# Performance work log

Hardware: AMD Instinct MI355X
Metric: run time of the kernel (lower is better)

Reference implementation:

```python
import jax, jax.numpy as jnp
import numpy as np

CONF_THRES = 0.2   # from __init__ default
IOU_THRES = 0.6    # from __init__ default
MAX_WH = 4096.0    # class-offset for multi-class NMS (yolov7 convention)
TOPK = 2048        # pre-NMS candidates per image
MAX_DET = 300      # max detections per image (yolov7 default)
B, N, NC = 8, 25200, 80


def setup_inputs() -> dict:
    key = jax.random.key(0)
    k1, k2, k3 = jax.random.split(key, 3)
    # decoded predictions: [cx, cy, w, h, obj, cls_0..cls_79]
    xywh = jax.random.uniform(k1, (B, N, 4)) * jnp.array([640.0, 640.0, 120.0, 120.0])
    obj = jax.random.uniform(k2, (B, N, 1))
    cls = jax.random.uniform(k3, (B, N, NC))
    preds = jnp.concatenate([xywh, obj, cls], axis=-1)  # [B, N, 85]
    return {"preds": preds}


def _xywh2xyxy(xywh):
    cx, cy, w, h = xywh[..., 0], xywh[..., 1], xywh[..., 2], xywh[..., 3]
    return jnp.stack([cx - w * 0.5, cy - h * 0.5, cx + w * 0.5, cy + h * 0.5], axis=-1)


def _box_iou(a, b):
    # a: [K,4], b: [K,4] -> [K,K] pairwise IoU
    area_a = (a[:, 2] - a[:, 0]) * (a[:, 3] - a[:, 1])
    area_b = (b[:, 2] - b[:, 0]) * (b[:, 3] - b[:, 1])
    lt = jnp.maximum(a[:, None, :2], b[None, :, :2])  # [K,K,2]
    rb = jnp.minimum(a[:, None, 2:], b[None, :, 2:])
    wh = jnp.clip(rb - lt, 0.0)
    inter = wh[..., 0] * wh[..., 1]
    return inter / (area_a[:, None] + area_b[None, :] - inter + 1e-9)


def _nms_single(pred):
    # pred: [N, 5+NC]
    boxes = _xywh2xyxy(pred[:, :4])                 # [N,4]
    scores_all = pred[:, 5:] * pred[:, 4:5]         # obj * cls  [N,NC]
    conf = jnp.max(scores_all, axis=-1)             # best-class conf
    cls_id = jnp.argmax(scores_all, axis=-1)
    scores = jnp.where(conf > CONF_THRES, conf, 0.0)

    # pre-NMS top-k candidates (sorted descending)
    top_scores, idx = jax.lax.top_k(scores, TOPK)
    top_boxes = boxes[idx]                          # [K,4]
    top_cls = cls_id[idx]                           # [K]
    top_valid = top_scores > CONF_THRES

    # per-class NMS via class offset so cross-class boxes never overlap
    offset_boxes = top_boxes + (top_cls.astype(top_boxes.dtype) * MAX_WH)[:, None]
    iou = _box_iou(offset_boxes, offset_boxes)      # [K,K]

    # greedy NMS over score-sorted candidates
    def body(i, state):
        keep, suppressed = state
        k_i = top_valid[i] & jnp.logical_not(suppressed[i])
        keep = keep.at[i].set(k_i)
        sup_new = suppressed | (k_i & (iou[i] > IOU_THRES))
        sup_new = sup_new.at[i].set(suppressed[i])  # never self-suppress
        return keep, sup_new

    keep, _ = jax.lax.fori_loop(
        0, TOPK, body,
        (jnp.zeros(TOPK, dtype=bool), jnp.zeros(TOPK, dtype=bool)))

    # take top MAX_DET kept detections
    keep_scores = jnp.where(keep, top_scores, -1.0)
    det_scores, det_idx = jax.lax.top_k(keep_scores, MAX_DET)
    det = jnp.concatenate(
        [top_boxes[det_idx],
         det_scores[:, None],
         top_cls[det_idx].astype(pred.dtype)[:, None]], axis=-1)  # [MAX_DET,6]
    det = jnp.where((det_scores > 0.0)[:, None], det, 0.0)
    return det


def reference(preds):
    # preds: [B, N, 5+NC] -> [B, MAX_DET, 6] (x1,y1,x2,y2,conf,cls), zero-padded
    return jax.vmap(_nms_single)(preds)
```

## Files before the change

kernel.cpp:

```cpp
#include <hip/hip_runtime.h>

#define BATCH 8
#define NPRED 25200
#define NCLS 80
#define ROWW 85
#define TOPKK 2048
#define MAXDET 300
#define CANDMAX 4096
#define NBUCKET 4096
#define CONF_T 0.2f
#define IOU_T 0.6f
#define CLS_OFF 4096.0f

#define MASKN 384
#define MCH (MASKN / 64)
#define MW 13

typedef unsigned long long u64;
typedef unsigned int u32;

__device__ __forceinline__ int bucket_of_key(u64 k) {
    float sc = __uint_as_float((u32)(k >> 32));
    int bkt = (int)(sc * (float)NBUCKET);
    return (bkt > NBUCKET - 1) ? (NBUCKET - 1) : bkt;
}

__global__ __launch_bounds__(256) void k_score(
    const float* __restrict__ preds,
    u64* __restrict__ keys,
    unsigned char* __restrict__ cls8,
    u32* __restrict__ hist_g)
{
    __shared__ float rows[64 * ROWW];
    const int t = threadIdx.x;
    const size_t rowbase = (size_t)blockIdx.x * 64;

    const float4* src = reinterpret_cast<const float4*>(preds + rowbase * ROWW);
    float4* dst = reinterpret_cast<float4*>(rows);
    #pragma unroll
    for (int i = t; i < 64 * ROWW / 4; i += 256) dst[i] = src[i];
    __syncthreads();

    const int r = t >> 2;
    const int j = t & 3;
    const float* p = rows + r * ROWW;
    const float obj = p[4];

    float best = -1.0f;
    int bi = 0;
    #pragma unroll
    for (int tt = 0; tt < 20; ++tt) {
        int c = j + 4 * tt;
        float s = __fmul_rn(obj, p[5 + c]);
        if (s > best) { best = s; bi = c; }
    }
    #pragma unroll
    for (int d = 1; d <= 2; d <<= 1) {
        float os = __shfl_xor(best, d);
        int oi = __shfl_xor(bi, d);
        if (os > best || (os == best && oi < bi)) { best = os; bi = oi; }
    }

    if (j == 0) {
        unsigned gid = (unsigned)rowbase + r;
        u64 key = 0ull;
        if (best > CONF_T) {
            key = ((u64)__float_as_uint(best) << 32) | (0xFFFFFFFFu - (gid % NPRED));
        }
        keys[gid] = key;
        cls8[gid] = (unsigned char)bi;
        if (key) {
            atomicAdd(&hist_g[(gid / NPRED) * NBUCKET + bucket_of_key(key)], 1u);
        }
    }
}

__global__ __launch_bounds__(1024) void k_scan(
    const u32* __restrict__ hist_g,
    u32* __restrict__ bstart_g,
    int* __restrict__ tb_g,
    u32* __restrict__ stored_g)
{
    __shared__ u32 wtot[16];
    __shared__ u32 wsuf[16];
    __shared__ int s_tb;
    __shared__ u32 s_stored;

    const int b = blockIdx.x;
    const int t = threadIdx.x;
    const int lane = t & 63;
    const int wave = t >> 6;
    const u32* H = hist_g + (size_t)b * NBUCKET;

    u32 h0 = H[4 * t], h1 = H[4 * t + 1], h2 = H[4 * t + 2], h3 = H[4 * t + 3];
    u32 ps = h0 + h1 + h2 + h3;

    u32 v = ps;
    #pragma unroll
    for (int off = 1; off < 64; off <<= 1) {
        u32 u2 = __shfl_down(v, off);
        if (lane + off < 64) v += u2;
    }
    if (lane == 0) wtot[wave] = v;
    __syncthreads();
    if (t < 16) {
        u32 w = wtot[t];
        u32 s = w;
        #pragma unroll
        for (int off = 1; off < 16; off <<= 1) {
            u32 u2 = __shfl_down(s, off);
            if (t + off < 16) s += u2;
        }
        wsuf[t] = s - w;
    }
    __syncthreads();
    u32 suffix_t = v + wsuf[wave];
    u32 snext = suffix_t - ps;

    u32 b3 = snext;
    u32 b2 = b3 + h3;
    u32 b1 = b2 + h2;
    u32 b0 = b1 + h1;
    u32* BS = bstart_g + (size_t)b * NBUCKET;
    BS[4 * t + 0] = b0;
    BS[4 * t + 1] = b1;
    BS[4 * t + 2] = b2;
    BS[4 * t + 3] = b3;

    if (t == 0) {
        s_tb = 0;
        s_stored = (suffix_t < (u32)CANDMAX) ? suffix_t : (u32)CANDMAX;
    }
    __syncthreads();
    {
        u32 c3 = b3 + h3, c2 = b2 + h2, c1 = b1 + h1, c0 = b0 + h0;
        if (c3 >= TOPKK && b3 < TOPKK) { s_tb = 4 * t + 3; s_stored = (c3 < (u32)CANDMAX) ? c3 : (u32)CANDMAX; }
        if (c2 >= TOPKK && b2 < TOPKK) { s_tb = 4 * t + 2; s_stored = (c2 < (u32)CANDMAX) ? c2 : (u32)CANDMAX; }
        if (c1 >= TOPKK && b1 < TOPKK) { s_tb = 4 * t + 1; s_stored = (c1 < (u32)CANDMAX) ? c1 : (u32)CANDMAX; }
        if (c0 >= TOPKK && b0 < TOPKK) { s_tb = 4 * t + 0; s_stored = (c0 < (u32)CANDMAX) ? c0 : (u32)CANDMAX; }
    }
    __syncthreads();
    if (t == 0) { tb_g[b] = s_tb; stored_g[b] = s_stored; }
}

__global__ __launch_bounds__(256) void k_compact(
    const u64* __restrict__ keys,
    const u32* __restrict__ bstart_g,
    u32* __restrict__ bfill_g,
    const int* __restrict__ tb_g,
    u64* __restrict__ cand_g)
{
    unsigned gid = blockIdx.x * 256 + threadIdx.x;
    if (gid >= BATCH * NPRED) return;
    u64 k = keys[gid];
    if (!k) return;
    int b = gid / NPRED;
    int bkt = bucket_of_key(k);
    if (bkt < tb_g[b]) return;
    u32 slot = bstart_g[(size_t)b * NBUCKET + bkt] +
               atomicAdd(&bfill_g[(size_t)b * NBUCKET + bkt], 1u);
    if (slot < CANDMAX) cand_g[(size_t)b * CANDMAX + slot] = k;
}

struct RankPhase {
    u32 histL[NBUCKET];
    u32 bstartL[NBUCKET];
};
struct NmsPhase {
    u32 masks32[MASKN * MW];
    float4 cbx[MASKN];
    float carea[MASKN];
    float4 kb[MAXDET];
};

__global__ __launch_bounds__(1024) void k_finish(
    const float* __restrict__ preds,
    const unsigned char* __restrict__ cls8,
    const u32* __restrict__ hist_g,
    const u32* __restrict__ bstart_g,
    const u32* __restrict__ stored_g,
    const u64* __restrict__ cand_g,
    float* __restrict__ out)
{
    __shared__ union { RankPhase rk; NmsPhase nms; } u;
    __shared__ u64 candL[CANDMAX];
    __shared__ unsigned short rank2cand[TOPKK];
    __shared__ float4 sbox[MASKN];
    __shared__ float sscore[MASKN];
    __shared__ float scls[MASKN];
    __shared__ u64 validw[MCH];

    const int b = blockIdx.x;
    const int t = threadIdx.x;
    const int lane = t & 63;
    const int wave = t >> 6;
    float* ob = out + (size_t)b * MAXDET * 6;
    const u32 stored = stored_g[b];

    for (int i = t; i < NBUCKET; i += 1024) {
        u.rk.histL[i] = hist_g[(size_t)b * NBUCKET + i];
        u.rk.bstartL[i] = bstart_g[(size_t)b * NBUCKET + i];
    }
    for (int i = t; i < TOPKK; i += 1024) rank2cand[i] = 0xFFFFu;
    for (int i = t; i < CANDMAX; i += 1024)
        if ((u32)i < stored) candL[i] = cand_g[(size_t)b * CANDMAX + i];
    if (t < MASKN) {
        sbox[t] = make_float4(0.f, 0.f, 0.f, 0.f);
        sscore[t] = 0.f;
        scls[t] = 0.f;
    }
    __syncthreads();

    for (u32 i = t; i < stored; i += 1024) {
        u64 k = candL[i];
        int bkt = bucket_of_key(k);
        u32 base = u.rk.bstartL[bkt];
        u32 end = base + u.rk.histL[bkt];
        if (end > stored) end = stored;
        u32 r = base;
        for (u32 jx = base; jx < end; ++jx) r += (candL[jx] > k) ? 1u : 0u;
        if (r < TOPKK) rank2cand[r] = (unsigned short)i;
        if (r < MASKN) {
            float sc = __uint_as_float((u32)(k >> 32));
            unsigned idx = 0xFFFFFFFFu - (u32)(k & 0xFFFFFFFFu);
            const float* p = preds + ((size_t)b * NPRED + idx) * ROWW;
            float cx = p[0], cy = p[1], w = p[2], h = p[3];
            float hw = __fmul_rn(w, 0.5f);
            float hh = __fmul_rn(h, 0.5f);
            sbox[r] = make_float4(__fsub_rn(cx, hw), __fsub_rn(cy, hh),
                                  __fadd_rn(cx, hw), __fadd_rn(cy, hh));
            sscore[r] = sc;
            scls[r] = (float)cls8[(size_t)b * NPRED + idx];
        }
    }
    __syncthreads();

    if (t < MASKN) {
        float sc = sscore[t];
        float cl = scls[t];
        float4 bb = sbox[t];
        float off = __fmul_rn(cl, CLS_OFF);
        float4 obx = make_float4(__fadd_rn(bb.x, off), __fadd_rn(bb.y, off),
                                 __fadd_rn(bb.z, off), __fadd_rn(bb.w, off));
        u.nms.cbx[t] = obx;
        u.nms.carea[t] = __fmul_rn(__fsub_rn(obx.z, obx.x), __fsub_rn(obx.w, obx.y));
        u64 vb = __ballot(sc > CONF_T);
        if (lane == 0) validw[wave] = vb;
    }
    __syncthreads();

    for (int tu = 0; tu < 3; ++tu) {
        int uidx = wave + 16 * tu;
        if (uidx >= 42) break;
        int q, s;
        if (uidx < 12)      { q = 0; s = uidx; }
        else if (uidx < 22) { q = 1; s = uidx - 12 + 2; }
        else if (uidx < 30) { q = 2; s = uidx - 22 + 4; }
        else if (uidx < 36) { q = 3; s = uidx - 30 + 6; }
        else if (uidx < 40) { q = 4; s = uidx - 36 + 8; }
        else                { q = 5; s = uidx - 40 + 10; }

        const int r = q * 64 + lane;
        const float4 me = u.nms.cbx[r];
        const float aA = u.nms.carea[r];
        const int j0 = s * 32;
        u32 acc = 0u;
        #pragma unroll 8
        for (int jj = 0; jj < 32; ++jj) {
            const int jx = j0 + jj;
            float4 cb = u.nms.cbx[jx];
            float lx = fmaxf(me.x, cb.x), ly = fmaxf(me.y, cb.y);
            float rx = fminf(me.z, cb.z), ry = fminf(me.w, cb.w);
            float iw = fmaxf(__fsub_rn(rx, lx), 0.0f);
            float ih = fmaxf(__fsub_rn(ry, ly), 0.0f);
            float inter = __fmul_rn(iw, ih);
            float denom = __fadd_rn(__fsub_rn(__fadd_rn(aA, u.nms.carea[jx]), inter), 1e-9f);
            bool sv = inter > __fmul_rn(IOU_T, denom);
            acc |= ((u32)sv) << jj;
        }
        if (s == 2 * q || s == 2 * q + 1) {
            int shift = r - j0;
            u32 dm = (shift < 0) ? ~0u : ((shift >= 31) ? 0u : (~0u << (shift + 1)));
            acc &= dm;
        }
        u.nms.masks32[r * MW + s] = acc;
    }
    __syncthreads();
    if (wave != 0) return;

    const u64 below = (lane == 0) ? 0ull : (~0ull >> (64 - lane));
    u64 S[MCH];
    #pragma unroll
    for (int w = 0; w < MCH; ++w) S[w] = 0ull;
    int nk = 0;
    bool done = false, allfull = true;

    #pragma unroll
    for (int c = 0; c < MCH; ++c) {
        if (done) break;
        u64 vw = validw[c];
        u64 eligible = vw & ~S[c];
        const int rbase = (c * 64 + lane) * MW;
        u64 Mu = ((u64)u.nms.masks32[rbase + 2 * c + 1] << 32) |
                 (u64)u.nms.masks32[rbase + 2 * c];
        bool elig = (eligible >> lane) & 1ull;
        if (eligible) {
            int cap = MAXDET - nk;
            u64 edge = __ballot(elig && ((Mu & eligible) != 0ull));
            u64 keptm;
            if (edge == 0ull) {
                int rank = __popcll(eligible & below);
                keptm = __ballot(elig && (rank < cap));
            } else {
                u64 km = 0ull, supm = 0ull;
                int cnt = 0;
                for (int m = 0; m < 64 && cnt < cap; ++m) {
                    if (!((eligible >> m) & 1ull)) continue;
                    if ((supm >> m) & 1ull) continue;
                    km |= 1ull << m;
                    ++cnt;
                    supm |= __shfl(Mu, m);
                }
                keptm = km;
            }
            if ((keptm >> lane) & 1ull) {
                int pos = nk + __popcll(keptm & below);
                int i = c * 64 + lane;
                float4 bb = sbox[i];
                u.nms.kb[pos] = u.nms.cbx[i];
                float* row = ob + pos * 6;
                row[0] = bb.x; row[1] = bb.y; row[2] = bb.z; row[3] = bb.w;
                row[4] = sscore[i]; row[5] = scls[i];
            }
            nk += __popcll(keptm);
            if (nk >= MAXDET) {
                done = true;
            } else if (keptm) {
                for (int w = c + 1; w < MCH; ++w) {
                    u64 v = ((keptm >> lane) & 1ull)
                        ? (((u64)u.nms.masks32[rbase + 2 * w + 1] << 32) |
                           (u64)u.nms.masks32[rbase + 2 * w])
                        : 0ull;
                    v |= __shfl_xor(v, 1);  v |= __shfl_xor(v, 2);
                    v |= __shfl_xor(v, 4);  v |= __shfl_xor(v, 8);
                    v |= __shfl_xor(v, 16); v |= __shfl_xor(v, 32);
                    S[w] |= v;
                }
            }
        }
        if (vw != ~0ull) { allfull = false; break; }
    }

    if (!done && allfull && nk < MAXDET) {
        __threadfence_block();
        for (int c = MCH; c < TOPKK / 64; ++c) {
            int r = c * 64 + lane;
            unsigned short ci = rank2cand[r];
            bool valid = (ci != 0xFFFFu);
            u64 validmask = __ballot(valid);
            if (validmask == 0ull) break;

            float sc = 0.f, cl = 0.f;
            float bx1 = 0.f, by1 = 0.f, bx2 = 0.f, by2 = 0.f;
            if (valid) {
                u64 k = candL[ci];
                sc = __uint_as_float((u32)(k >> 32));
                unsigned idx = 0xFFFFFFFFu - (u32)(k & 0xFFFFFFFFu);
                const float* p = preds + ((size_t)b * NPRED + idx) * ROWW;
                float cx = p[0], cy = p[1], w = p[2], h = p[3];
                float hw = __fmul_rn(w, 0.5f);
                float hh = __fmul_rn(h, 0.5f);
                bx1 = __fsub_rn(cx, hw); by1 = __fsub_rn(cy, hh);
                bx2 = __fadd_rn(cx, hw); by2 = __fadd_rn(cy, hh);
                cl = (float)cls8[(size_t)b * NPRED + idx];
            }
            float off = __fmul_rn(cl, CLS_OFF);
            float x1 = __fadd_rn(bx1, off), y1 = __fadd_rn(by1, off);
            float x2 = __fadd_rn(bx2, off), y2 = __fadd_rn(by2, off);
            float areaA = __fmul_rn(__fsub_rn(x2, x1), __fsub_rn(y2, y1));

            bool sup = false;
            for (int jx = 0; jx < nk; ++jx) {
                float4 k4 = u.nms.kb[jx];
                float lx = fmaxf(x1, k4.x), ly = fmaxf(y1, k4.y);
                float rx = fminf(x2, k4.z), ry = fminf(y2, k4.w);
                float iw = fmaxf(__fsub_rn(rx, lx), 0.0f);
                float ih = fmaxf(__fsub_rn(ry, ly), 0.0f);
                float inter = __fmul_rn(iw, ih);
                float areaB = __fmul_rn(__fsub_rn(k4.z, k4.x), __fsub_rn(k4.w, k4.y));
                float denom = __fadd_rn(__fsub_rn(__fadd_rn(areaA, areaB), inter), 1e-9f);
                if (inter > __fmul_rn(IOU_T, denom)) sup = true;
            }
            u64 supprev = __ballot(sup);

            u32 sb_lo = 0u, sb_hi = 0u;
            for (int m = 0; m < 64; ++m) {
                float mx1 = __shfl(x1, m), my1 = __shfl(y1, m);
                float mx2 = __shfl(x2, m), my2 = __shfl(y2, m);
                float lx = fmaxf(x1, mx1), ly = fmaxf(y1, my1);
                float rx = fminf(x2, mx2), ry = fminf(y2, my2);
                float iw = fmaxf(__fsub_rn(rx, lx), 0.0f);
                float ih = fmaxf(__fsub_rn(ry, ly), 0.0f);
                float inter = __fmul_rn(iw, ih);
                float areaB = __fmul_rn(__fsub_rn(mx2, mx1), __fsub_rn(my2, my1));
                float denom = __fadd_rn(__fsub_rn(__fadd_rn(areaA, areaB), inter), 1e-9f);
                bool s = (m != lane) && (inter > __fmul_rn(IOU_T, denom));
                if (m < 32) sb_lo |= ((u32)s) << m;
                else        sb_hi |= ((u32)s) << (m - 32);
            }

            u64 eligible = validmask & ~supprev;
            u64 mysb = (((u64)sb_hi << 32) | (u64)sb_lo);
            bool iselig = (eligible >> lane) & 1ull;
            u64 edgeball = __ballot(iselig && ((mysb & eligible & below) != 0ull));

            u64 keptm;
            int cap = MAXDET - nk;
            if (edgeball == 0ull) {
                int rank = __popcll(eligible & below);
                keptm = __ballot(iselig && (rank < cap));
            } else {
                u64 km = 0ull;
                int cnt = 0;
                for (int m = 0; m < 64 && cnt < cap; ++m) {
                    if (!((validmask >> m) & 1ull)) break;
                    if ((supprev >> m) & 1ull) continue;
                    u32 mlo = (u32)__shfl((int)sb_lo, m);
                    u32 mhi = (u32)__shfl((int)sb_hi, m);
                    u64 supby = (((u64)mhi << 32) | (u64)mlo);
                    if (supby & km) continue;
                    km |= 1ull << m;
                    ++cnt;
                }
                keptm = km;
            }

            if ((keptm >> lane) & 1ull) {
                int pos = nk + __popcll(keptm & below);
                u.nms.kb[pos] = make_float4(x1, y1, x2, y2);
                float* row = ob + pos * 6;
                row[0] = bx1; row[1] = by1; row[2] = bx2; row[3] = by2;
                row[4] = sc;  row[5] = cl;
            }
            __threadfence_block();
            nk += __popcll(keptm);
            if (nk >= MAXDET) break;
            if (validmask != ~0ull) break;
        }
    }

    for (int x = nk * 6 + lane; x < MAXDET * 6; x += 64) ob[x] = 0.0f;
}

extern "C" void kernel_launch(void* const* d_in, const int* in_sizes, int n_in,
                              void* d_out, int out_size, void* d_ws, size_t ws_size,
                              hipStream_t stream) {
    const float* preds = (const float*)d_in[0];
    float* out = (float*)d_out;

    u32* hist_g   = (u32*)d_ws;
    u32* bfill_g  = hist_g + BATCH * NBUCKET;
    u32* bstart_g = bfill_g + BATCH * NBUCKET;
    int* tb_g     = (int*)(bstart_g + BATCH * NBUCKET);
    u32* stored_g = (u32*)(tb_g + 8);
    u64* keys     = (u64*)(stored_g + 8);
    unsigned char* cls8 = (unsigned char*)(keys + BATCH * NPRED);
    u64* cand_g   = (u64*)(cls8 + BATCH * NPRED);

    hipMemsetAsync(hist_g, 0, (size_t)2 * BATCH * NBUCKET * sizeof(u32), stream);

    hipLaunchKernelGGL(k_score, dim3(BATCH * NPRED / 64), dim3(256), 0, stream,
                       preds, keys, cls8, hist_g);
    hipLaunchKernelGGL(k_scan, dim3(BATCH), dim3(1024), 0, stream,
                       hist_g, bstart_g, tb_g, stored_g);
    hipLaunchKernelGGL(k_compact, dim3((BATCH * NPRED + 255) / 256), dim3(256), 0, stream,
                       keys, bstart_g, bfill_g, tb_g, cand_g);
    hipLaunchKernelGGL(k_finish, dim3(BATCH), dim3(1024), 0, stream,
                       preds, cls8, hist_g, bstart_g, stored_g, cand_g, out);
}
```

Baseline: 69.33 us.

## Build per-image histogram in scan kernel shared memory, drop global atomics and memset

The score kernel no longer does global atomic histogram updates. Instead, the scan kernel (one block per image) rereads the keys and builds the histogram with shared-memory atomics. This removes the memset launch and the contended global atomics. The compact kernel now uses a prefilled allocation array, so it needs one atomic instead of a load plus an atomic. The finish kernel loads only buckets at or above the threshold bucket. The cost is that 8 blocks each serially read about 200KB of keys, so the scan kernel now has very little parallelism.

```diff
diff --git a/kernel.cpp b/kernel.cpp
--- a/kernel.cpp
+++ b/kernel.cpp
@@ -28,8 +28,7 @@
 __global__ __launch_bounds__(256) void k_score(
     const float* __restrict__ preds,
     u64* __restrict__ keys,
-    unsigned char* __restrict__ cls8,
-    u32* __restrict__ hist_g)
+    unsigned char* __restrict__ cls8)
 {
     __shared__ float rows[64 * ROWW];
     const int t = threadIdx.x;
@@ -69,18 +68,18 @@
         }
         keys[gid] = key;
         cls8[gid] = (unsigned char)bi;
-        if (key) {
-            atomicAdd(&hist_g[(gid / NPRED) * NBUCKET + bucket_of_key(key)], 1u);
-        }
     }
 }
 
 __global__ __launch_bounds__(1024) void k_scan(
-    const u32* __restrict__ hist_g,
+    const u64* __restrict__ keys,
+    u32* __restrict__ hist_g,
     u32* __restrict__ bstart_g,
+    u32* __restrict__ balloc_g,
     int* __restrict__ tb_g,
     u32* __restrict__ stored_g)
 {
+    __shared__ u32 histL[NBUCKET];
     __shared__ u32 wtot[16];
     __shared__ u32 wsuf[16];
     __shared__ int s_tb;
@@ -90,9 +89,18 @@
     const int t = threadIdx.x;
     const int lane = t & 63;
     const int wave = t >> 6;
-    const u32* H = hist_g + (size_t)b * NBUCKET;
-
-    u32 h0 = H[4 * t], h1 = H[4 * t + 1], h2 = H[4 * t + 2], h3 = H[4 * t + 3];
+    const u64* bk = keys + (size_t)b * NPRED;
+
+    for (int i = t; i < NBUCKET; i += 1024) histL[i] = 0u;
+    __syncthreads();
+
+    for (int i = t; i < NPRED; i += 1024) {
+        u64 k = bk[i];
+        if (k) atomicAdd(&histL[bucket_of_key(k)], 1u);
+    }
+    __syncthreads();
+
+    u32 h0 = histL[4 * t], h1 = histL[4 * t + 1], h2 = histL[4 * t + 2], h3 = histL[4 * t + 3];
     u32 ps = h0 + h1 + h2 + h3;
 
     u32 v = ps;
@@ -121,11 +129,19 @@
     u32 b2 = b3 + h3;
     u32 b1 = b2 + h2;
     u32 b0 = b1 + h1;
-    u32* BS = bstart_g + (size_t)b * NBUCKET;
-    BS[4 * t + 0] = b0;
-    BS[4 * t + 1] = b1;
-    BS[4 * t + 2] = b2;
-    BS[4 * t + 3] = b3;
+    const size_t B0 = (size_t)b * NBUCKET;
+    hist_g[B0 + 4 * t + 0] = h0;
+    hist_g[B0 + 4 * t + 1] = h1;
+    hist_g[B0 + 4 * t + 2] = h2;
+    hist_g[B0 + 4 * t + 3] = h3;
+    bstart_g[B0 + 4 * t + 0] = b0;
+    bstart_g[B0 + 4 * t + 1] = b1;
+    bstart_g[B0 + 4 * t + 2] = b2;
+    bstart_g[B0 + 4 * t + 3] = b3;
+    balloc_g[B0 + 4 * t + 0] = b0;
+    balloc_g[B0 + 4 * t + 1] = b1;
+    balloc_g[B0 + 4 * t + 2] = b2;
+    balloc_g[B0 + 4 * t + 3] = b3;
 
     if (t == 0) {
         s_tb = 0;
@@ -145,8 +161,7 @@
 
 __global__ __launch_bounds__(256) void k_compact(
     const u64* __restrict__ keys,
-    const u32* __restrict__ bstart_g,
-    u32* __restrict__ bfill_g,
+    u32* __restrict__ balloc_g,
     const int* __restrict__ tb_g,
     u64* __restrict__ cand_g)
 {
@@ -157,8 +172,7 @@
     int b = gid / NPRED;
     int bkt = bucket_of_key(k);
     if (bkt < tb_g[b]) return;
-    u32 slot = bstart_g[(size_t)b * NBUCKET + bkt] +
-               atomicAdd(&bfill_g[(size_t)b * NBUCKET + bkt], 1u);
+    u32 slot = atomicAdd(&balloc_g[(size_t)b * NBUCKET + bkt], 1u);
     if (slot < CANDMAX) cand_g[(size_t)b * CANDMAX + slot] = k;
 }
 
@@ -178,6 +192,7 @@
     const unsigned char* __restrict__ cls8,
     const u32* __restrict__ hist_g,
     const u32* __restrict__ bstart_g,
+    const int* __restrict__ tb_g,
     const u32* __restrict__ stored_g,
     const u64* __restrict__ cand_g,
     float* __restrict__ out)
@@ -196,8 +211,9 @@
     const int wave = t >> 6;
     float* ob = out + (size_t)b * MAXDET * 6;
     const u32 stored = stored_g[b];
-
-    for (int i = t; i < NBUCKET; i += 1024) {
+    const int tb = tb_g[b];
+
+    for (int i = tb + t; i < NBUCKET; i += 1024) {
         u.rk.histL[i] = hist_g[(size_t)b * NBUCKET + i];
         u.rk.bstartL[i] = bstart_g[(size_t)b * NBUCKET + i];
     }
@@ -459,22 +475,20 @@
     float* out = (float*)d_out;
 
     u32* hist_g   = (u32*)d_ws;
-    u32* bfill_g  = hist_g + BATCH * NBUCKET;
-    u32* bstart_g = bfill_g + BATCH * NBUCKET;
-    int* tb_g     = (int*)(bstart_g + BATCH * NBUCKET);
+    u32* bstart_g = hist_g + BATCH * NBUCKET;
+    u32* balloc_g = bstart_g + BATCH * NBUCKET;
+    int* tb_g     = (int*)(balloc_g + BATCH * NBUCKET);
     u32* stored_g = (u32*)(tb_g + 8);
     u64* keys     = (u64*)(stored_g + 8);
     unsigned char* cls8 = (unsigned char*)(keys + BATCH * NPRED);
     u64* cand_g   = (u64*)(cls8 + BATCH * NPRED);
 
-    hipMemsetAsync(hist_g, 0, (size_t)2 * BATCH * NBUCKET * sizeof(u32), stream);
-
     hipLaunchKernelGGL(k_score, dim3(BATCH * NPRED / 64), dim3(256), 0, stream,
-                       preds, keys, cls8, hist_g);
+                       preds, keys, cls8);
     hipLaunchKernelGGL(k_scan, dim3(BATCH), dim3(1024), 0, stream,
-                       hist_g, bstart_g, tb_g, stored_g);
+                       keys, hist_g, bstart_g, balloc_g, tb_g, stored_g);
     hipLaunchKernelGGL(k_compact, dim3((BATCH * NPRED + 255) / 256), dim3(256), 0, stream,
-                       keys, bstart_g, bfill_g, tb_g, cand_g);
+                       keys, balloc_g, tb_g, cand_g);
     hipLaunchKernelGGL(k_finish, dim3(BATCH), dim3(1024), 0, stream,
-                       preds, cls8, hist_g, bstart_g, stored_g, cand_g, out);
-}
+                       preds, cls8, hist_g, bstart_g, tb_g, stored_g, cand_g, out);
+}
```

After: 67.29 us. 1.03x faster.
